# Kernel tuning notes

Hardware: AMD Instinct MI355X
Metric: run time of the kernel (lower is better)

Reference implementation:

```python
import jax, jax.numpy as jnp
import numpy as np

B, T, C = 8, 4096, 256
N_LAYER, LAYER_ID = 12, 5


def setup_inputs() -> dict:
    key = jax.random.key(0)
    ks = jax.random.split(key, 5)
    x = jax.random.normal(ks[0], (B, T, C), dtype=jnp.float32)
    scale = 1.0 / np.sqrt(C)
    Wk = jax.random.normal(ks[1], (C, C), jnp.float32) * scale
    Wv = jax.random.normal(ks[2], (C, C), jnp.float32) * scale
    Wr = jax.random.normal(ks[3], (C, C), jnp.float32) * scale
    Wo = jax.random.normal(ks[4], (C, C), jnp.float32) * scale
    # 'fancy' init from _init_weights
    ratio_0_to_1 = LAYER_ID / (N_LAYER - 1)
    h = np.arange(C, dtype=np.float64)
    decay = -5.0 + 8.0 * (h / (C - 1)) ** (0.7 + 1.3 * ratio_0_to_1)
    zigzag = ((np.arange(C) + 1) % 3 - 1) * 0.5
    first = np.log(0.3) + zigzag
    return dict(
        x=x, Wk=Wk, Wv=Wv, Wr=Wr, Wo=Wo,
        spatial_decay=jnp.asarray(decay, jnp.float32),
        spatial_first=jnp.asarray(first, jnp.float32),
        ln_w=jnp.ones((C,), jnp.float32),
        ln_b=jnp.zeros((C,), jnp.float32),
    )


def _wkv(w, u, k, v):
    # Numerically-stable RWKV WKV scan, matching wkv_cuda forward.
    # w, u: [C] (already divided by T); k, v: [B, T, C]. Returns y: [B, T, C].
    MIN_VALUE = -1e38

    def step(carry, kv):
        p, q, o = carry            # [B, C] each
        kt, vt = kv                # [B, C]
        no = jnp.maximum(o, u + kt)
        a = jnp.exp(o - no)
        b = jnp.exp(u + kt - no)
        y = (a * p + b * vt) / (a * q + b)
        no2 = jnp.maximum(w + o, kt)
        a2 = jnp.exp(w + o - no2)
        b2 = jnp.exp(kt - no2)
        return (a2 * p + b2 * vt, a2 * q + b2, no2), y

    p0 = jnp.zeros(k.shape[0:1] + k.shape[2:3], k.dtype)  # [B, C]
    q0 = jnp.zeros_like(p0)
    o0 = jnp.full_like(p0, MIN_VALUE)
    kT = jnp.swapaxes(k, 0, 1)  # [T, B, C]
    vT = jnp.swapaxes(v, 0, 1)
    _, yT = jax.lax.scan(step, (p0, q0, o0), (kT, vT))
    return jnp.swapaxes(yT, 0, 1)


def _layernorm(x, w, b, eps=1e-5):
    mu = jnp.mean(x, axis=-1, keepdims=True)
    xc = x - mu
    var = jnp.mean(xc * xc, axis=-1, keepdims=True)
    return xc * jax.lax.rsqrt(var + eps) * w + b


def reference(x, Wk, Wv, Wr, Wo, spatial_decay, spatial_first, ln_w, ln_b):
    # shift_pixel == 0 -> xk = xv = xr = x (module's own code path)
    t = x.shape[1]
    k = jnp.einsum('btc,dc->btd', x, Wk)
    v = jnp.einsum('btc,dc->btd', x, Wv)
    r = jnp.einsum('btc,dc->btd', x, Wr)
    sr = jax.nn.sigmoid(r)
    y = _wkv(spatial_decay / t, spatial_first / t, k, v)
    y = _layernorm(y, ln_w, ln_b)
    return jnp.einsum('btc,dc->btd', sr * y, Wo)
```

## Files before the change

### kernel.cpp

```cpp
#include <hip/hip_runtime.h>
#include <cstdint>
#include <cstddef>

#define B_ 8
#define T_ 4096
#define C_ 256
#define NC_ 256
#define L_ (T_ / NC_)
#define M_ (B_ * T_)

typedef float f32x4 __attribute__((ext_vector_type(4)));
typedef short bf16x8 __attribute__((ext_vector_type(8)));

__device__ __forceinline__ unsigned short f2b(float f) {
    unsigned int u = __float_as_uint(f);
    u += 0x7fffu + ((u >> 16) & 1u);
    return (unsigned short)(u >> 16);
}
__device__ __forceinline__ float b2f(unsigned short h) {
    return __uint_as_float(((unsigned int)h) << 16);
}

__global__ __launch_bounds__(256) void cvt_all(const float* __restrict__ x,
                                               const float* __restrict__ Wk,
                                               const float* __restrict__ Wv,
                                               const float* __restrict__ Wr,
                                               const float* __restrict__ Wo,
                                               unsigned short* __restrict__ xb,
                                               unsigned short* __restrict__ wb) {
    const int bid = blockIdx.x;
    const float* src;
    unsigned short* dst;
    size_t base;
    if (bid < 4096) {
        src = x; dst = xb;
        base = (size_t)bid * 2048;
    } else {
        const int r = bid - 4096;
        const int mat = r >> 5;
        src = (mat == 0) ? Wk : (mat == 1) ? Wv : (mat == 2) ? Wr : Wo;
        dst = wb + (size_t)mat * 65536;
        base = (size_t)(r & 31) * 2048;
    }
    const size_t i = base + (size_t)threadIdx.x * 8;
    float4 a = *(const float4*)(src + i);
    float4 b = *(const float4*)(src + i + 4);
    bf16x8 o;
    o[0] = (short)f2b(a.x); o[1] = (short)f2b(a.y);
    o[2] = (short)f2b(a.z); o[3] = (short)f2b(a.w);
    o[4] = (short)f2b(b.x); o[5] = (short)f2b(b.y);
    o[6] = (short)f2b(b.z); o[7] = (short)f2b(b.w);
    *(bf16x8*)(dst + i) = o;
}

__global__ __launch_bounds__(256, 3) void gemm_qkv(const unsigned short* __restrict__ A,
                                                   const unsigned short* __restrict__ w0,
                                                   const unsigned short* __restrict__ w1,
                                                   const unsigned short* __restrict__ w2,
                                                   float* __restrict__ f0,
                                                   float* __restrict__ f1,
                                                   unsigned short* __restrict__ b2) {
    __shared__ unsigned short wlds[64 * 264];
    __shared__ float stage[4][16 * 68];
    const int tid = threadIdx.x;
    const int wave = tid >> 6, lane = tid & 63;
    const int quad = lane >> 4, l16 = lane & 15;
    const int m0 = blockIdx.x * 128 + wave * 32;
    const int n0 = blockIdx.y * 64;
    float* myst = stage[wave];

    bf16x8 af[2][8];
#pragma unroll
    for (int mt = 0; mt < 2; ++mt) {
        const unsigned short* Ar = A + (size_t)(m0 + mt * 16 + l16) * C_ + quad * 8;
#pragma unroll
        for (int kc = 0; kc < 8; ++kc) af[mt][kc] = *(const bf16x8*)(Ar + kc * 32);
    }

    const int r = tid >> 5;
    const int cs = (tid & 31) * 8;

    for (int mat = 0; mat < 3; ++mat) {
        const unsigned short* W = (mat == 0) ? w0 : (mat == 1) ? w1 : w2;
        bf16x8 tmp[8];
#pragma unroll
        for (int it = 0; it < 8; ++it)
            tmp[it] = *(const bf16x8*)(W + (size_t)(n0 + it * 8 + r) * C_ + cs);
        __syncthreads();
#pragma unroll
        for (int it = 0; it < 8; ++it)
            *(bf16x8*)(wlds + (it * 8 + r) * 264 + cs) = tmp[it];
        __syncthreads();

#pragma unroll
        for (int mt = 0; mt < 2; ++mt) {
            f32x4 acc[4];
#pragma unroll
            for (int nt = 0; nt < 4; ++nt) acc[nt] = (f32x4){0.f, 0.f, 0.f, 0.f};
#pragma unroll
            for (int nt = 0; nt < 4; ++nt) {
                const unsigned short* wrow = wlds + (nt * 16 + l16) * 264 + quad * 8;
#pragma unroll
                for (int kc = 0; kc < 8; ++kc) {
                    bf16x8 wf = *(const bf16x8*)(wrow + kc * 32);
                    acc[nt] = __builtin_amdgcn_mfma_f32_16x16x32_bf16(af[mt][kc], wf, acc[nt], 0, 0, 0);
                }
            }

#pragma unroll
            for (int nt = 0; nt < 4; ++nt)
#pragma unroll
                for (int i = 0; i < 4; ++i)
                    myst[(quad * 4 + i) * 68 + nt * 16 + l16] = acc[nt][i];
#pragma unroll
            for (int rr = 0; rr < 4; ++rr) {
                const int row = rr * 4 + quad;
                float4 t4 = *(const float4*)&myst[row * 68 + l16 * 4];
                const size_t gidx = (size_t)(m0 + mt * 16 + row) * C_ + n0 + l16 * 4;
                if (mat == 0) {
                    *(float4*)(f0 + gidx) = t4;
                } else if (mat == 1) {
                    *(float4*)(f1 + gidx) = t4;
                } else {
                    ushort4 s4;
                    s4.x = f2b(1.f / (1.f + __expf(-t4.x)));
                    s4.y = f2b(1.f / (1.f + __expf(-t4.y)));
                    s4.z = f2b(1.f / (1.f + __expf(-t4.z)));
                    s4.w = f2b(1.f / (1.f + __expf(-t4.w)));
                    *(ushort4*)(b2 + gidx) = s4;
                }
            }
        }
    }
}

__global__ __launch_bounds__(256, 3) void gemm_out(const unsigned short* __restrict__ A,
                                                   const unsigned short* __restrict__ w0,
                                                   float* __restrict__ f0) {
    __shared__ unsigned short wlds[64 * 264];
    __shared__ float stage[4][16 * 68];
    const int tid = threadIdx.x;
    const int wave = tid >> 6, lane = tid & 63;
    const int quad = lane >> 4, l16 = lane & 15;
    const int m0 = blockIdx.x * 128 + wave * 32;
    const int n0 = blockIdx.y * 64;
    float* myst = stage[wave];

    {
        const int r = tid >> 5;
        const int cs = (tid & 31) * 8;
        bf16x8 tmp[8];
#pragma unroll
        for (int it = 0; it < 8; ++it)
            tmp[it] = *(const bf16x8*)(w0 + (size_t)(n0 + it * 8 + r) * C_ + cs);
#pragma unroll
        for (int it = 0; it < 8; ++it)
            *(bf16x8*)(wlds + (it * 8 + r) * 264 + cs) = tmp[it];
    }
    __syncthreads();

#pragma unroll
    for (int mt = 0; mt < 2; ++mt) {
        const unsigned short* Ar = A + (size_t)(m0 + mt * 16 + l16) * C_ + quad * 8;
        bf16x8 af[8];
#pragma unroll
        for (int kc = 0; kc < 8; ++kc) af[kc] = *(const bf16x8*)(Ar + kc * 32);

        f32x4 acc[4];
#pragma unroll
        for (int nt = 0; nt < 4; ++nt) acc[nt] = (f32x4){0.f, 0.f, 0.f, 0.f};
#pragma unroll
        for (int nt = 0; nt < 4; ++nt) {
            const unsigned short* wrow = wlds + (nt * 16 + l16) * 264 + quad * 8;
#pragma unroll
            for (int kc = 0; kc < 8; ++kc) {
                bf16x8 wf = *(const bf16x8*)(wrow + kc * 32);
                acc[nt] = __builtin_amdgcn_mfma_f32_16x16x32_bf16(af[kc], wf, acc[nt], 0, 0, 0);
            }
        }

#pragma unroll
        for (int nt = 0; nt < 4; ++nt)
#pragma unroll
            for (int i = 0; i < 4; ++i)
                myst[(quad * 4 + i) * 68 + nt * 16 + l16] = acc[nt][i];
#pragma unroll
        for (int rr = 0; rr < 4; ++rr) {
            const int row = rr * 4 + quad;
            float4 t4 = *(const float4*)&myst[row * 68 + l16 * 4];
            *(float4*)(f0 + (size_t)(m0 + mt * 16 + row) * C_ + n0 + l16 * 4) = t4;
        }
    }
}

__global__ __launch_bounds__(256) void wkv_pass1(const float* __restrict__ k,
                                                 const float* __restrict__ v,
                                                 const float* __restrict__ decay,
                                                 float* __restrict__ sp, float* __restrict__ sq,
                                                 float* __restrict__ so) {
    const int c = threadIdx.x, chunk = blockIdx.x, b = blockIdx.y;
    const float w = decay[c] * (1.0f / T_);
    size_t base = ((size_t)b * T_ + (size_t)chunk * L_) * C_ + c;
    float p = 0.f, q = 0.f, o = -1e38f;
    for (int t = 0; t < L_; t += 8) {
        float kk[8], vv[8];
#pragma unroll
        for (int j = 0; j < 8; ++j) {
            kk[j] = k[base + (size_t)(t + j) * C_];
            vv[j] = v[base + (size_t)(t + j) * C_];
        }
#pragma unroll
        for (int j = 0; j < 8; ++j) {
            float wo = w + o;
            float no = fmaxf(wo, kk[j]);
            float a2 = __expf(wo - no), b2 = __expf(kk[j] - no);
            p = a2 * p + b2 * vv[j];
            q = a2 * q + b2;
            o = no;
        }
    }
    size_t idx = ((size_t)b * NC_ + chunk) * C_ + c;
    sp[idx] = p; sq[idx] = q; so[idx] = o;
}

__global__ __launch_bounds__(256) void wkv_combine_par(const float* __restrict__ decay,
                                                       float* __restrict__ sp,
                                                       float* __restrict__ sq,
                                                       float* __restrict__ so) {
    __shared__ float tp[16][17], tq[16][17], to[16][17];
    const int tid = threadIdx.x;
    const int cg = tid >> 4;
    const int cl = tid & 15;
    const int b = blockIdx.x;
    const int c = blockIdx.y * 16 + cl;
    const float wL = decay[c] * (1.0f / T_) * (float)L_;
    const float wL16 = wL * 16.0f;
    const size_t base = ((size_t)b * NC_ + (size_t)cg * 16) * C_ + c;

    float p = 0.f, q = 0.f, o = -1e38f;
#pragma unroll 4
    for (int j = 0; j < 16; ++j) {
        size_t idx = base + (size_t)j * C_;
        float lp = sp[idx], lq = sq[idx], lo = so[idx];
        float ow = o + wL;
        float no = fmaxf(ow, lo);
        float ea = __expf(ow - no), eb = __expf(lo - no);
        p = ea * p + eb * lp;
        q = ea * q + eb * lq;
        o = no;
    }
    tp[cg][cl] = p; tq[cg][cl] = q; to[cg][cl] = o;

    float ip = p, iq = q, io = o;
#pragma unroll
    for (int off = 1; off < 16; off <<= 1) {
        __syncthreads();
        float ap = 0.f, aq = 0.f, ao = 0.f;
        const bool doit = (cg >= off);
        if (doit) { ap = tp[cg - off][cl]; aq = tq[cg - off][cl]; ao = to[cg - off][cl]; }
        __syncthreads();
        if (doit) {
            float ow = ao + (float)off * wL16;
            float no = fmaxf(ow, io);
            float ea = __expf(ow - no), eb = __expf(io - no);
            ip = ea * ap + eb * ip;
            iq = ea * aq + eb * iq;
            io = no;
            tp[cg][cl] = ip; tq[cg][cl] = iq; to[cg][cl] = io;
        }
    }
    __syncthreads();

    float ep, eq, eo;
    if (cg == 0) { ep = 0.f; eq = 0.f; eo = -1e38f; }
    else         { ep = tp[cg - 1][cl]; eq = tq[cg - 1][cl]; eo = to[cg - 1][cl]; }

    for (int j = 0; j < 16; ++j) {
        size_t idx = base + (size_t)j * C_;
        float lp = sp[idx], lq = sq[idx], lo = so[idx];
        sp[idx] = ep; sq[idx] = eq; so[idx] = eo;
        float ow = eo + wL;
        float no = fmaxf(ow, lo);
        float ea = __expf(ow - no), eb = __expf(lo - no);
        ep = ea * ep + eb * lp;
        eq = ea * eq + eb * lq;
        eo = no;
    }
}

__global__ __launch_bounds__(256, 8) void wkv_pass2_ln(const float* __restrict__ k,
                                                       const float* __restrict__ v,
                                                       const unsigned short* __restrict__ sr,
                                                       const float* __restrict__ decay,
                                                       const float* __restrict__ first,
                                                       const float* __restrict__ lw,
                                                       const float* __restrict__ lb,
                                                       const float* __restrict__ sp,
                                                       const float* __restrict__ sq,
                                                       const float* __restrict__ so,
                                                       unsigned short* __restrict__ z) {
    __shared__ float tile[16][264];
    __shared__ float mu_s[16], rs_s[16];
    const int c = threadIdx.x, chunk = blockIdx.x, b = blockIdx.y;
    const int wave = c >> 6, lane = c & 63;
    const float w = decay[c] * (1.0f / T_);
    const float u = first[c] * (1.0f / T_);
    const float gw = lw[c], gb = lb[c];
    size_t sidx = ((size_t)b * NC_ + chunk) * C_ + c;
    float p = sp[sidx], q = sq[sidx], o = so[sidx];
    size_t base = ((size_t)b * T_ + (size_t)chunk * L_) * C_ + c;

    for (int t = 0; t < L_; t += 8) {
        float kk[8], vv[8];
#pragma unroll
        for (int j = 0; j < 8; ++j) {
            kk[j] = k[base + (size_t)(t + j) * C_];
            vv[j] = v[base + (size_t)(t + j) * C_];
        }
#pragma unroll
        for (int j = 0; j < 8; ++j) {
            float uk = u + kk[j];
            float no = fmaxf(o, uk);
            float a = __expf(o - no), bb = __expf(uk - no);
            tile[t + j][c] = (a * p + bb * vv[j]) / (a * q + bb);
            float wo = w + o;
            float no2 = fmaxf(wo, kk[j]);
            float a2 = __expf(wo - no2), b2 = __expf(kk[j] - no2);
            p = a2 * p + b2 * vv[j];
            q = a2 * q + b2;
            o = no2;
        }
    }
    __syncthreads();
#pragma unroll
    for (int r = 0; r < 4; ++r) {
        const int j = wave * 4 + r;
        float4 t4 = *(const float4*)&tile[j][lane * 4];
        float s = t4.x + t4.y + t4.z + t4.w;
        float ss = t4.x * t4.x + t4.y * t4.y + t4.z * t4.z + t4.w * t4.w;
#pragma unroll
        for (int m = 1; m < 64; m <<= 1) {
            s += __shfl_xor(s, m, 64);
            ss += __shfl_xor(ss, m, 64);
        }
        if (lane == 0) {
            float mu = s * (1.f / C_);
            mu_s[j] = mu;
            rs_s[j] = rsqrtf(ss * (1.f / C_) - mu * mu + 1e-5f);
        }
    }
    __syncthreads();
#pragma unroll
    for (int j = 0; j < L_; ++j) {
        float zz = (tile[j][c] - mu_s[j]) * rs_s[j] * gw + gb;
        zz *= b2f(sr[base + (size_t)j * C_]);
        z[base + (size_t)j * C_] = f2b(zz);
    }
}

extern "C" void kernel_launch(void* const* d_in, const int* in_sizes, int n_in,
                              void* d_out, int out_size, void* d_ws, size_t ws_size,
                              hipStream_t stream) {
    const float* x     = (const float*)d_in[0];
    const float* Wk    = (const float*)d_in[1];
    const float* Wv    = (const float*)d_in[2];
    const float* Wr    = (const float*)d_in[3];
    const float* Wo    = (const float*)d_in[4];
    const float* decay = (const float*)d_in[5];
    const float* first = (const float*)d_in[6];
    const float* lnw   = (const float*)d_in[7];
    const float* lnb   = (const float*)d_in[8];
    float* out = (float*)d_out;

    char* ws = (char*)d_ws;
    const size_t NE = (size_t)M_ * C_;
    unsigned short* wb  = (unsigned short*)ws; ws += 4 * 65536 * 2;
    unsigned short* xb  = (unsigned short*)ws; ws += NE * 2;
    float* kbuf = (float*)ws; ws += NE * 4;
    float* vbuf = (float*)ws; ws += NE * 4;
    unsigned short* srb = (unsigned short*)ws; ws += NE * 2;
    unsigned short* zb  = (unsigned short*)ws; ws += NE * 2;
    const size_t SE = (size_t)B_ * NC_ * C_;
    float* sp = (float*)ws; ws += SE * 4;
    float* sq = (float*)ws; ws += SE * 4;
    float* so = (float*)ws; ws += SE * 4;
    unsigned short* wkb = wb;
    unsigned short* wvb = wb + 65536;
    unsigned short* wrb = wb + 2 * 65536;
    unsigned short* wob = wb + 3 * 65536;

    cvt_all<<<4096 + 128, 256, 0, stream>>>(x, Wk, Wv, Wr, Wo, xb, wb);

    gemm_qkv<<<dim3(M_ / 128, 4), 256, 0, stream>>>(xb, wkb, wvb, wrb,
                                                    kbuf, vbuf, srb);

    wkv_pass1<<<dim3(NC_, B_), 256, 0, stream>>>(kbuf, vbuf, decay, sp, sq, so);
    wkv_combine_par<<<dim3(B_, C_ / 16), 256, 0, stream>>>(decay, sp, sq, so);
    wkv_pass2_ln<<<dim3(NC_, B_), 256, 0, stream>>>(kbuf, vbuf, srb, decay, first,
                                                    lnw, lnb, sp, sq, so, zb);

    gemm_out<<<dim3(M_ / 128, 4), 256, 0, stream>>>(zb, wob, out);
}
```

Before: 179.5 us.

## Drop LDS epilogue staging, prefetch next weight matrix, raise occupancy hint

Result: slower. 188.9 us (+5.3%).

```diff
diff --git a/kernel.cpp b/kernel.cpp
--- a/kernel.cpp
+++ b/kernel.cpp
@@ -53,7 +53,7 @@
     *(bf16x8*)(dst + i) = o;
 }
 
-__global__ __launch_bounds__(256, 3) void gemm_qkv(const unsigned short* __restrict__ A,
+__global__ __launch_bounds__(256, 4) void gemm_qkv(const unsigned short* __restrict__ A,
                                                    const unsigned short* __restrict__ w0,
                                                    const unsigned short* __restrict__ w1,
                                                    const unsigned short* __restrict__ w2,
@@ -61,13 +61,11 @@
                                                    float* __restrict__ f1,
                                                    unsigned short* __restrict__ b2) {
     __shared__ unsigned short wlds[64 * 264];
-    __shared__ float stage[4][16 * 68];
     const int tid = threadIdx.x;
     const int wave = tid >> 6, lane = tid & 63;
     const int quad = lane >> 4, l16 = lane & 15;
     const int m0 = blockIdx.x * 128 + wave * 32;
     const int n0 = blockIdx.y * 64;
-    float* myst = stage[wave];
 
     bf16x8 af[2][8];
 #pragma unroll
@@ -80,17 +78,24 @@
     const int r = tid >> 5;
     const int cs = (tid & 31) * 8;
 
+    bf16x8 tmp[8];
+#pragma unroll
+    for (int it = 0; it < 8; ++it)
+        tmp[it] = *(const bf16x8*)(w0 + (size_t)(n0 + it * 8 + r) * C_ + cs);
+
     for (int mat = 0; mat < 3; ++mat) {
-        const unsigned short* W = (mat == 0) ? w0 : (mat == 1) ? w1 : w2;
-        bf16x8 tmp[8];
-#pragma unroll
-        for (int it = 0; it < 8; ++it)
-            tmp[it] = *(const bf16x8*)(W + (size_t)(n0 + it * 8 + r) * C_ + cs);
         __syncthreads();
 #pragma unroll
         for (int it = 0; it < 8; ++it)
             *(bf16x8*)(wlds + (it * 8 + r) * 264 + cs) = tmp[it];
         __syncthreads();
+
+        if (mat < 2) {
+            const unsigned short* Wn = (mat == 0) ? w1 : w2;
+#pragma unroll
+            for (int it = 0; it < 8; ++it)
+                tmp[it] = *(const bf16x8*)(Wn + (size_t)(n0 + it * 8 + r) * C_ + cs);
+        }
 
 #pragma unroll
         for (int mt = 0; mt < 2; ++mt) {
@@ -106,45 +111,38 @@
                     acc[nt] = __builtin_amdgcn_mfma_f32_16x16x32_bf16(af[mt][kc], wf, acc[nt], 0, 0, 0);
                 }
             }
-
-#pragma unroll
-            for (int nt = 0; nt < 4; ++nt)
-#pragma unroll
-                for (int i = 0; i < 4; ++i)
-                    myst[(quad * 4 + i) * 68 + nt * 16 + l16] = acc[nt][i];
-#pragma unroll
-            for (int rr = 0; rr < 4; ++rr) {
-                const int row = rr * 4 + quad;
-                float4 t4 = *(const float4*)&myst[row * 68 + l16 * 4];
-                const size_t gidx = (size_t)(m0 + mt * 16 + row) * C_ + n0 + l16 * 4;
-                if (mat == 0) {
-                    *(float4*)(f0 + gidx) = t4;
-                } else if (mat == 1) {
-                    *(float4*)(f1 + gidx) = t4;
-                } else {
-                    ushort4 s4;
-                    s4.x = f2b(1.f / (1.f + __expf(-t4.x)));
-                    s4.y = f2b(1.f / (1.f + __expf(-t4.y)));
-                    s4.z = f2b(1.f / (1.f + __expf(-t4.z)));
-                    s4.w = f2b(1.f / (1.f + __expf(-t4.w)));
-                    *(ushort4*)(b2 + gidx) = s4;
-                }
+            if (mat == 2) {
+#pragma unroll
+                for (int nt = 0; nt < 4; ++nt)
+#pragma unroll
+                    for (int i = 0; i < 4; ++i) {
+                        const int row = m0 + mt * 16 + quad * 4 + i;
+                        float s = 1.f / (1.f + __expf(-acc[nt][i]));
+                        b2[(size_t)row * C_ + n0 + nt * 16 + l16] = f2b(s);
+                    }
+            } else {
+                float* F = (mat == 0) ? f0 : f1;
+#pragma unroll
+                for (int nt = 0; nt < 4; ++nt)
+#pragma unroll
+                    for (int i = 0; i < 4; ++i) {
+                        const int row = m0 + mt * 16 + quad * 4 + i;
+                        F[(size_t)row * C_ + n0 + nt * 16 + l16] = acc[nt][i];
+                    }
             }
         }
     }
 }
 
-__global__ __launch_bounds__(256, 3) void gemm_out(const unsigned short* __restrict__ A,
+__global__ __launch_bounds__(256, 4) void gemm_out(const unsigned short* __restrict__ A,
                                                    const unsigned short* __restrict__ w0,
                                                    float* __restrict__ f0) {
     __shared__ unsigned short wlds[64 * 264];
-    __shared__ float stage[4][16 * 68];
     const int tid = threadIdx.x;
     const int wave = tid >> 6, lane = tid & 63;
     const int quad = lane >> 4, l16 = lane & 15;
     const int m0 = blockIdx.x * 128 + wave * 32;
     const int n0 = blockIdx.y * 64;
-    float* myst = stage[wave];
 
     {
         const int r = tid >> 5;
@@ -178,18 +176,13 @@
                 acc[nt] = __builtin_amdgcn_mfma_f32_16x16x32_bf16(af[kc], wf, acc[nt], 0, 0, 0);
             }
         }
-
 #pragma unroll
         for (int nt = 0; nt < 4; ++nt)
 #pragma unroll
-            for (int i = 0; i < 4; ++i)
-                myst[(quad * 4 + i) * 68 + nt * 16 + l16] = acc[nt][i];
-#pragma unroll
-        for (int rr = 0; rr < 4; ++rr) {
-            const int row = rr * 4 + quad;
-            float4 t4 = *(const float4*)&myst[row * 68 + l16 * 4];
-            *(float4*)(f0 + (size_t)(m0 + mt * 16 + row) * C_ + n0 + l16 * 4) = t4;
-        }
+            for (int i = 0; i < 4; ++i) {
+                const int row = m0 + mt * 16 + quad * 4 + i;
+                f0[(size_t)row * C_ + n0 + nt * 16 + l16] = acc[nt][i];
+            }
     }
 }
 
```

## Fuse x bf16 conversion into QKV GEMM and prefetch next weight tile

Applied to the files above, without the earlier changes.

Result: slower. 191.5 us (+6.7%).

```diff
diff --git a/kernel.cpp b/kernel.cpp
--- a/kernel.cpp
+++ b/kernel.cpp
@@ -21,28 +21,16 @@
     return __uint_as_float(((unsigned int)h) << 16);
 }
 
-__global__ __launch_bounds__(256) void cvt_all(const float* __restrict__ x,
-                                               const float* __restrict__ Wk,
-                                               const float* __restrict__ Wv,
-                                               const float* __restrict__ Wr,
-                                               const float* __restrict__ Wo,
-                                               unsigned short* __restrict__ xb,
-                                               unsigned short* __restrict__ wb) {
-    const int bid = blockIdx.x;
-    const float* src;
-    unsigned short* dst;
-    size_t base;
-    if (bid < 4096) {
-        src = x; dst = xb;
-        base = (size_t)bid * 2048;
-    } else {
-        const int r = bid - 4096;
-        const int mat = r >> 5;
-        src = (mat == 0) ? Wk : (mat == 1) ? Wv : (mat == 2) ? Wr : Wo;
-        dst = wb + (size_t)mat * 65536;
-        base = (size_t)(r & 31) * 2048;
-    }
-    const size_t i = base + (size_t)threadIdx.x * 8;
+__global__ __launch_bounds__(256) void cvt_w(const float* __restrict__ Wk,
+                                             const float* __restrict__ Wv,
+                                             const float* __restrict__ Wr,
+                                             const float* __restrict__ Wo,
+                                             unsigned short* __restrict__ wb) {
+    const int r = blockIdx.x;
+    const int mat = r >> 5;
+    const float* src = (mat == 0) ? Wk : (mat == 1) ? Wv : (mat == 2) ? Wr : Wo;
+    unsigned short* dst = wb + (size_t)mat * 65536;
+    const size_t i = (size_t)(r & 31) * 2048 + (size_t)threadIdx.x * 8;
     float4 a = *(const float4*)(src + i);
     float4 b = *(const float4*)(src + i + 4);
     bf16x8 o;
@@ -53,7 +41,7 @@
     *(bf16x8*)(dst + i) = o;
 }
 
-__global__ __launch_bounds__(256, 3) void gemm_qkv(const unsigned short* __restrict__ A,
+__global__ __launch_bounds__(256, 3) void gemm_qkv(const float* __restrict__ x,
                                                    const unsigned short* __restrict__ w0,
                                                    const unsigned short* __restrict__ w1,
                                                    const unsigned short* __restrict__ w2,
@@ -72,25 +60,41 @@
     bf16x8 af[2][8];
 #pragma unroll
     for (int mt = 0; mt < 2; ++mt) {
-        const unsigned short* Ar = A + (size_t)(m0 + mt * 16 + l16) * C_ + quad * 8;
-#pragma unroll
-        for (int kc = 0; kc < 8; ++kc) af[mt][kc] = *(const bf16x8*)(Ar + kc * 32);
+        const float* Ar = x + (size_t)(m0 + mt * 16 + l16) * C_ + quad * 8;
+#pragma unroll
+        for (int kc = 0; kc < 8; ++kc) {
+            float4 a = *(const float4*)(Ar + kc * 32);
+            float4 b = *(const float4*)(Ar + kc * 32 + 4);
+            bf16x8 o;
+            o[0] = (short)f2b(a.x); o[1] = (short)f2b(a.y);
+            o[2] = (short)f2b(a.z); o[3] = (short)f2b(a.w);
+            o[4] = (short)f2b(b.x); o[5] = (short)f2b(b.y);
+            o[6] = (short)f2b(b.z); o[7] = (short)f2b(b.w);
+            af[mt][kc] = o;
+        }
     }
 
     const int r = tid >> 5;
     const int cs = (tid & 31) * 8;
 
+    bf16x8 tmp[8];
+#pragma unroll
+    for (int it = 0; it < 8; ++it)
+        tmp[it] = *(const bf16x8*)(w0 + (size_t)(n0 + it * 8 + r) * C_ + cs);
+
     for (int mat = 0; mat < 3; ++mat) {
-        const unsigned short* W = (mat == 0) ? w0 : (mat == 1) ? w1 : w2;
-        bf16x8 tmp[8];
-#pragma unroll
-        for (int it = 0; it < 8; ++it)
-            tmp[it] = *(const bf16x8*)(W + (size_t)(n0 + it * 8 + r) * C_ + cs);
         __syncthreads();
 #pragma unroll
         for (int it = 0; it < 8; ++it)
             *(bf16x8*)(wlds + (it * 8 + r) * 264 + cs) = tmp[it];
         __syncthreads();
+
+        if (mat < 2) {
+            const unsigned short* Wn = (mat == 0) ? w1 : w2;
+#pragma unroll
+            for (int it = 0; it < 8; ++it)
+                tmp[it] = *(const bf16x8*)(Wn + (size_t)(n0 + it * 8 + r) * C_ + cs);
+        }
 
 #pragma unroll
         for (int mt = 0; mt < 2; ++mt) {
@@ -375,7 +379,6 @@
     char* ws = (char*)d_ws;
     const size_t NE = (size_t)M_ * C_;
     unsigned short* wb  = (unsigned short*)ws; ws += 4 * 65536 * 2;
-    unsigned short* xb  = (unsigned short*)ws; ws += NE * 2;
     float* kbuf = (float*)ws; ws += NE * 4;
     float* vbuf = (float*)ws; ws += NE * 4;
     unsigned short* srb = (unsigned short*)ws; ws += NE * 2;
@@ -389,9 +392,9 @@
     unsigned short* wrb = wb + 2 * 65536;
     unsigned short* wob = wb + 3 * 65536;
 
-    cvt_all<<<4096 + 128, 256, 0, stream>>>(x, Wk, Wv, Wr, Wo, xb, wb);
-
-    gemm_qkv<<<dim3(M_ / 128, 4), 256, 0, stream>>>(xb, wkb, wvb, wrb,
+    cvt_w<<<128, 256, 0, stream>>>(Wk, Wv, Wr, Wo, wb);
+
+    gemm_qkv<<<dim3(M_ / 128, 4), 256, 0, stream>>>(x, wkb, wvb, wrb,
                                                     kbuf, vbuf, srb);
 
     wkv_pass1<<<dim3(NC_, B_), 256, 0, stream>>>(kbuf, vbuf, decay, sp, sq, so);
```
